# Kernel tuning notes

Hardware: AMD Instinct MI355X
Metric: run time of the kernel (lower is better)

## Reference

```python
import jax, jax.numpy as jnp
import numpy as np

NEG_INF = -9e15
ALPHA = 0.2  # LeakyReLU negative slope

N = 8192
D_IN = 512
D_OUT = 256


def setup_inputs() -> dict:
    key = jax.random.key(0)
    k1, k2, k3, k4, k5 = jax.random.split(key, 5)
    features = jax.random.normal(k1, (N, D_IN), dtype=jnp.float32)
    adjacency_matrix = jax.random.randint(k2, (N, N), 0, 2, dtype=jnp.int32)
    # learned params (torch Linear stores [out, in]; we use [in, out] layout)
    s_phi = 1.0 / np.sqrt(D_IN)
    W_phi = jax.random.uniform(k3, (D_IN, D_OUT), jnp.float32, -s_phi, s_phi)
    s_v = 1.0 / np.sqrt(D_OUT)
    w_mu = jax.random.uniform(k4, (D_OUT,), jnp.float32, -s_v, s_v)
    w_xi = jax.random.uniform(k5, (D_OUT,), jnp.float32, -s_v, s_v)
    return {"features": features, "adjacency_matrix": adjacency_matrix,
            "W_phi": W_phi, "w_mu": w_mu, "w_xi": w_xi}


def reference(features, adjacency_matrix, W_phi, w_mu, w_xi):
    h = features @ W_phi                                   # [N, d_out]
    mu = h @ w_mu                                          # [N]
    xi = h @ w_xi                                          # [N]
    e = mu[:, None] + xi[None, :]                          # [N, N] additive scores
    e = jnp.where(e >= 0, e, ALPHA * e)                    # LeakyReLU
    e = jnp.where(adjacency_matrix > 0, e, NEG_INF)        # mask non-edges
    a = jax.nn.softmax(e, axis=1)                          # row softmax (dropout p=0)
    out = a @ h                                            # weighted aggregation
    return jax.nn.elu(out)
```

## Files before the change

### kernel.cpp

```cpp
#include <hip/hip_runtime.h>
#include <cstdint>
#include <cstddef>


#define LOG2E 1.44269504f

typedef __attribute__((ext_vector_type(8))) short short8;
typedef __attribute__((ext_vector_type(4))) float floatx4;

using uint_as1 = __attribute__((address_space(1))) unsigned int;
using uint_as3 = __attribute__((address_space(3))) unsigned int;

__device__ __forceinline__ void gld_lds16(const void* g, void* l) {
  __builtin_amdgcn_global_load_lds((const uint_as1*)g, (uint_as3*)l, 16, 0, 0);
}

__device__ __forceinline__ unsigned short f2b(float f) {
  unsigned u = __float_as_uint(f);
  u += 0x7fffu + ((u >> 16) & 1u);
  return (unsigned short)(u >> 16);
}
__device__ __forceinline__ float b2f(short s) {
  return __uint_as_float(((unsigned)(unsigned short)s) << 16);
}

__global__ void k_bitmask(const int* __restrict__ adj, unsigned long long* __restrict__ bm) {
  int gw = (blockIdx.x * 256 + threadIdx.x) >> 6;
  int lane = threadIdx.x & 63;
  size_t w0 = (size_t)gw * 128;
  for (int r = 0; r < 128; r += 4) {
    size_t wd = w0 + r;
    int v0 = adj[(wd + 0) * 64 + lane];
    int v1 = adj[(wd + 1) * 64 + lane];
    int v2 = adj[(wd + 2) * 64 + lane];
    int v3 = adj[(wd + 3) * 64 + lane];
    unsigned long long m0 = __ballot(v0 != 0);
    unsigned long long m1 = __ballot(v1 != 0);
    unsigned long long m2 = __ballot(v2 != 0);
    unsigned long long m3 = __ballot(v3 != 0);
    if (lane == 0) {
      bm[wd] = m0; bm[wd + 1] = m1; bm[wd + 2] = m2; bm[wd + 3] = m3;
    }
  }
}

__global__ void k_cvt_features(const float* __restrict__ f, unsigned short* __restrict__ fb) {
  int tid = blockIdx.x * 256 + threadIdx.x;
  float4 v = ((const float4*)f)[tid];
  ushort4 o = {f2b(v.x), f2b(v.y), f2b(v.z), f2b(v.w)};
  *(ushort4*)&fb[tid * 4] = o;
}

__global__ void k_prep_wt(const float* __restrict__ w, unsigned short* __restrict__ wt) {
  int tid = blockIdx.x * 256 + threadIdx.x;
  int n = tid >> 9, k = tid & 511;
  wt[n * 512 + k] = f2b(w[k * 256 + n]);
}

__global__ void k_prep_p(const float* __restrict__ w, const float* __restrict__ wmu,
                         const float* __restrict__ wxi, float* __restrict__ pmu,
                         float* __restrict__ pxi) {
  int tid = blockIdx.x * 256 + threadIdx.x;
  int k = tid >> 2, seg = tid & 3;
  float sm = 0.f, sx = 0.f;
  int base = k * 256 + seg * 64;
#pragma unroll
  for (int c = 0; c < 64; c += 4) {
    float4 wv = *(const float4*)&w[base + c];
    float4 mv = *(const float4*)&wmu[seg * 64 + c];
    float4 xv = *(const float4*)&wxi[seg * 64 + c];
    sm += wv.x * mv.x + wv.y * mv.y + wv.z * mv.z + wv.w * mv.w;
    sx += wv.x * xv.x + wv.y * xv.y + wv.z * xv.z + wv.w * xv.w;
  }
  sm += __shfl_xor(sm, 1); sm += __shfl_xor(sm, 2);
  sx += __shfl_xor(sx, 1); sx += __shfl_xor(sx, 2);
  if (seg == 0) { pmu[k] = sm; pxi[k] = sx; }
}

__global__ void k_mu_xi(const unsigned short* __restrict__ fb, const float* __restrict__ pmu,
                        const float* __restrict__ pxi, float* __restrict__ mu,
                        float* __restrict__ xi) {
  int w = threadIdx.x >> 6, l = threadIdx.x & 63;
  int i = blockIdx.x * 4 + w;
  short8 fv = *(const short8*)&fb[i * 512 + l * 8];
  float m = 0.f, x = 0.f;
#pragma unroll
  for (int c = 0; c < 8; ++c) {
    float fvf = b2f(fv[c]);
    m = fmaf(fvf, pmu[l * 8 + c], m);
    x = fmaf(fvf, pxi[l * 8 + c], x);
  }
#pragma unroll
  for (int off = 32; off > 0; off >>= 1) {
    m += __shfl_xor(m, off);
    x += __shfl_xor(x, off);
  }
  if (l == 0) { mu[i] = m * LOG2E; xi[i] = x * LOG2E; }
}

__global__ __launch_bounds__(256, 2) void k_gemm1(const unsigned short* __restrict__ fb,
                                                  const unsigned short* __restrict__ wt,
                                                  unsigned short* __restrict__ ht) {
  __shared__ __align__(16) unsigned short As[64 * 64];
  __shared__ __align__(16) unsigned short Bs[128 * 64];
  int t = threadIdx.x, w = t >> 6, l = t & 63;
  int bm_ = blockIdx.x >> 1, bn = blockIdx.x & 1;
  int m0 = bm_ * 64, n0 = bn * 128;
  int lr = l >> 3, lg = l & 7, g = lg ^ lr;
  int kg = l >> 4, ln = l & 15;
  floatx4 zero = {0.f, 0.f, 0.f, 0.f};
  floatx4 acc[4][2];
#pragma unroll
  for (int mf = 0; mf < 4; ++mf)
#pragma unroll
    for (int nf = 0; nf < 2; ++nf) acc[mf][nf] = zero;

  for (int it = 0; it < 8; ++it) {
    int k0 = it * 64;
#pragma unroll
    for (int q = 0; q < 2; ++q) {
      int row = w * 16 + q * 8 + lr;
      const void* gp = fb + (size_t)(m0 + row) * 512 + k0 + g * 8;
      int lb = __builtin_amdgcn_readfirstlane((w * 16 + q * 8) * 64);
      gld_lds16(gp, &As[lb]);
    }
#pragma unroll
    for (int q = 0; q < 4; ++q) {
      int row = w * 32 + q * 8 + lr;
      const void* gp = wt + (size_t)(n0 + row) * 512 + k0 + g * 8;
      int lb = __builtin_amdgcn_readfirstlane((w * 32 + q * 8) * 64);
      gld_lds16(gp, &Bs[lb]);
    }
    __syncthreads();
#pragma unroll
    for (int ks = 0; ks < 2; ++ks) {
      int gg = ks * 4 + kg;
      int swz = (gg ^ (ln & 7)) * 8;
      short8 bfr[2];
#pragma unroll
      for (int nf = 0; nf < 2; ++nf)
        bfr[nf] = *(const short8*)&Bs[(w * 32 + nf * 16 + ln) * 64 + swz];
#pragma unroll
      for (int mf = 0; mf < 4; ++mf) {
        short8 afr = *(const short8*)&As[(mf * 16 + ln) * 64 + swz];
#pragma unroll
        for (int nf = 0; nf < 2; ++nf)
          acc[mf][nf] = __builtin_amdgcn_mfma_f32_16x16x32_bf16(afr, bfr[nf], acc[mf][nf], 0, 0, 0);
      }
    }
    __syncthreads();
  }
#pragma unroll
  for (int mf = 0; mf < 4; ++mf)
#pragma unroll
    for (int nf = 0; nf < 2; ++nf) {
      int ng = n0 + w * 32 + nf * 16 + ln;
      int mg = m0 + mf * 16 + kg * 4;
      ushort4 o = {f2b(acc[mf][nf][0]), f2b(acc[mf][nf][1]),
                   f2b(acc[mf][nf][2]), f2b(acc[mf][nf][3])};
      *(ushort4*)&ht[(size_t)ng * 8192 + mg] = o;
    }
}

__global__ void k_zero(float* __restrict__ num, float* __restrict__ zbuf) {
  int b = blockIdx.x, t = threadIdx.x;
  if (b < 2048) {
    float4 z4 = {0.f, 0.f, 0.f, 0.f};
    *(float4*)&num[(b * 256 + t) * 4] = z4;
  } else {
    zbuf[(b - 2048) * 256 + t] = 0.f;
  }
}

__global__ __launch_bounds__(256, 2) void k_attn5(const unsigned short* __restrict__ bm16,
                                                  const unsigned short* __restrict__ ht,
                                                  const float* __restrict__ mu,
                                                  const float* __restrict__ xi,
                                                  float* __restrict__ num,
                                                  float* __restrict__ zbuf) {
  __shared__ __align__(16) unsigned short Bs[2][256 * 64];
  __shared__ __align__(16) unsigned short Ws[64 * 64];

  int t = threadIdx.x, w = t >> 6, l = t & 63;
  int ln = l & 15, kg = l >> 4;
  int lr = l >> 3, lg = l & 7, g = lg ^ lr;
  int bi = blockIdx.x & 127, bj = blockIdx.x >> 7;
  int i0 = bi * 64;
  size_t jw = (size_t)bj * 2048;

  int wi = t >> 2;
  int js = (t & 3) * 16;
  int g0 = (t & 3) * 2;
  int p0i = (g0 ^ (wi & 7)) * 8;
  int p1i = ((g0 + 1) ^ (wi & 7)) * 8;
  float mu_s = mu[i0 + wi];
  const unsigned short* brow = bm16 + (size_t)(i0 + wi) * 512 + (jw + js) / 16;
  const float* xrow = xi + jw + js;
  float zacc = 0.f;

  floatx4 zero = {0.f, 0.f, 0.f, 0.f};
  floatx4 acc[4][4];
#pragma unroll
  for (int mf = 0; mf < 4; ++mf)
#pragma unroll
    for (int nf = 0; nf < 4; ++nf) acc[mf][nf] = zero;

  {
    unsigned bits = brow[0];
    float4 x0 = *(const float4*)(xrow + 0);
    float4 x1 = *(const float4*)(xrow + 4);
    float4 x2 = *(const float4*)(xrow + 8);
    float4 x3 = *(const float4*)(xrow + 12);
#pragma unroll
    for (int q = 0; q < 8; ++q) {
      int row = w * 64 + q * 8;
      const void* gp = ht + (size_t)(row + lr) * 8192 + jw + g * 8;
      int lb = __builtin_amdgcn_readfirstlane(row * 64);
      gld_lds16(gp, &Bs[0][lb]);
    }
    float xv[16] = {x0.x, x0.y, x0.z, x0.w, x1.x, x1.y, x1.z, x1.w,
                    x2.x, x2.y, x2.z, x2.w, x3.x, x3.y, x3.z, x3.w};
    short8 pk0, pk1;
#pragma unroll
    for (int e = 0; e < 16; ++e) {
      float s = mu_s + xv[e];
      s = fmaxf(s, 0.2f * s);
      float ev = __builtin_amdgcn_exp2f(s);
      float wv = (bits & (1u << e)) ? ev : 0.f;
      zacc += wv;
      if (e < 8) pk0[e] = (short)f2b(wv); else pk1[e - 8] = (short)f2b(wv);
    }
    *(short8*)&Ws[wi * 64 + p0i] = pk0;
    *(short8*)&Ws[wi * 64 + p1i] = pk1;
  }
  __syncthreads();

  for (int c = 0; c < 32; ++c) {
    int buf = c & 1, nb = buf ^ 1;
    float4 x0, x1, x2, x3;
    unsigned bits = 0;
    if (c < 31) {
      int jo1 = (c + 1) * 64;
#pragma unroll
      for (int q = 0; q < 8; ++q) {
        int row = w * 64 + q * 8;
        const void* gp = ht + (size_t)(row + lr) * 8192 + jw + jo1 + g * 8;
        int lb = __builtin_amdgcn_readfirstlane(nb * (256 * 64) + row * 64);
        gld_lds16(gp, &Bs[0][lb]);
      }
      bits = brow[(c + 1) * 4];
      x0 = *(const float4*)(xrow + jo1);
      x1 = *(const float4*)(xrow + jo1 + 4);
      x2 = *(const float4*)(xrow + jo1 + 8);
      x3 = *(const float4*)(xrow + jo1 + 12);
    }
#pragma unroll
    for (int ks = 0; ks < 2; ++ks) {
      int swz = ((ks * 4 + kg) ^ (ln & 7)) * 8;
      short8 af[4], bf[4];
#pragma unroll
      for (int mf = 0; mf < 4; ++mf)
        af[mf] = *(const short8*)&Ws[(mf * 16 + ln) * 64 + swz];
#pragma unroll
      for (int nf = 0; nf < 4; ++nf)
        bf[nf] = *(const short8*)&Bs[buf][(w * 64 + nf * 16 + ln) * 64 + swz];
#pragma unroll
      for (int mf = 0; mf < 4; ++mf)
#pragma unroll
        for (int nf = 0; nf < 4; ++nf)
          acc[mf][nf] = __builtin_amdgcn_mfma_f32_16x16x32_bf16(af[mf], bf[nf], acc[mf][nf], 0, 0, 0);
    }
    __syncthreads();
    if (c < 31) {
      float xv[16] = {x0.x, x0.y, x0.z, x0.w, x1.x, x1.y, x1.z, x1.w,
                      x2.x, x2.y, x2.z, x2.w, x3.x, x3.y, x3.z, x3.w};
      short8 pk0, pk1;
#pragma unroll
      for (int e = 0; e < 16; ++e) {
        float s = mu_s + xv[e];
        s = fmaxf(s, 0.2f * s);
        float ev = __builtin_amdgcn_exp2f(s);
        float wv = (bits & (1u << e)) ? ev : 0.f;
        zacc += wv;
        if (e < 8) pk0[e] = (short)f2b(wv); else pk1[e - 8] = (short)f2b(wv);
      }
      *(short8*)&Ws[wi * 64 + p0i] = pk0;
      *(short8*)&Ws[wi * 64 + p1i] = pk1;
    }
    __syncthreads();
  }

  zacc += __shfl_xor(zacc, 1);
  zacc += __shfl_xor(zacc, 2);
  if ((t & 3) == 0) atomicAdd(&zbuf[i0 + wi], zacc);

#pragma unroll
  for (int mf = 0; mf < 4; ++mf)
#pragma unroll
    for (int nf = 0; nf < 4; ++nf) {
      int col = w * 64 + nf * 16 + ln;
#pragma unroll
      for (int r = 0; r < 4; ++r) {
        int row = i0 + mf * 16 + kg * 4 + r;
        atomicAdd(&num[(size_t)row * 256 + col], acc[mf][nf][r]);
      }
    }
}

__global__ void k_final(const float* __restrict__ num, const float* __restrict__ zbuf,
                        float* __restrict__ out) {
  int tid = blockIdx.x * 256 + threadIdx.x;
  int i = tid >> 6;
  float zi = 1.0f / zbuf[i];
  float4 v = *(const float4*)&num[tid * 4];
  v.x *= zi; v.y *= zi; v.z *= zi; v.w *= zi;
  v.x = (v.x > 0.f) ? v.x : (__builtin_amdgcn_exp2f(v.x * LOG2E) - 1.f);
  v.y = (v.y > 0.f) ? v.y : (__builtin_amdgcn_exp2f(v.y * LOG2E) - 1.f);
  v.z = (v.z > 0.f) ? v.z : (__builtin_amdgcn_exp2f(v.z * LOG2E) - 1.f);
  v.w = (v.w > 0.f) ? v.w : (__builtin_amdgcn_exp2f(v.w * LOG2E) - 1.f);
  *(float4*)&out[tid * 4] = v;
}

extern "C" void kernel_launch(void* const* d_in, const int* in_sizes, int n_in,
                              void* d_out, int out_size, void* d_ws, size_t ws_size,
                              hipStream_t stream) {
  const float* features = (const float*)d_in[0];
  const int* adjm = (const int*)d_in[1];
  const float* W_phi = (const float*)d_in[2];
  const float* w_mu = (const float*)d_in[3];
  const float* w_xi = (const float*)d_in[4];
  float* out = (float*)d_out;

  char* ws = (char*)d_ws;
  unsigned short* fb  = (unsigned short*)(ws + 0);
  unsigned short* ht  = (unsigned short*)(ws + 8388608);
  unsigned short* wt  = (unsigned short*)(ws + 12582912);
  float* pmu = (float*)(ws + 12845056);
  float* pxi = (float*)(ws + 12847104);
  float* muv = (float*)(ws + 12849152);
  float* xiv = (float*)(ws + 12881920);
  unsigned long long* bmask = (unsigned long long*)(ws + 13631488);
  float* num  = (float*)(ws + 0);
  float* zbuf = (float*)(ws + 12582912);

  k_bitmask<<<2048, 256, 0, stream>>>(adjm, bmask);
  k_cvt_features<<<4096, 256, 0, stream>>>(features, fb);
  k_prep_wt<<<512, 256, 0, stream>>>(W_phi, wt);
  k_prep_p<<<8, 256, 0, stream>>>(W_phi, w_mu, w_xi, pmu, pxi);
  k_mu_xi<<<2048, 256, 0, stream>>>(fb, pmu, pxi, muv, xiv);
  k_gemm1<<<256, 256, 0, stream>>>(fb, wt, ht);
  k_zero<<<2080, 256, 0, stream>>>(num, zbuf);
  k_attn5<<<512, 256, 0, stream>>>((const unsigned short*)bmask, ht, muv, xiv, num, zbuf);
  k_final<<<2048, 256, 0, stream>>>(num, zbuf, out);
}
```

Baseline: 489.2 us.

## Factor exp of LeakyReLU scores into per-node products and drop atomics

Precomputes exp(mu), exp(0.2 mu), exp(xi) and exp(0.2 xi) per node. Each attention weight then becomes max(Emu*Exi, Fmu*Fxi), so the per-element exp disappears and the weights are built directly in MFMA A-fragments. The row-sum Z comes from an MFMA against a ones vector. Tiling changes to 256 rows by 128 columns over 1024-wide j chunks, and results go to per-chunk partial buffers reduced in k_final, which removes the zeroing kernel and the float atomics. In exchange it risks overflow or underflow without max subtraction, since the exponentials are computed separately before multiplying, and it adds more partial-buffer traffic.

```diff
diff --git a/kernel.cpp b/kernel.cpp
--- a/kernel.cpp
+++ b/kernel.cpp
@@ -78,8 +78,9 @@
 }
 
 __global__ void k_mu_xi(const unsigned short* __restrict__ fb, const float* __restrict__ pmu,
-                        const float* __restrict__ pxi, float* __restrict__ mu,
-                        float* __restrict__ xi) {
+                        const float* __restrict__ pxi, float* __restrict__ Emu,
+                        float* __restrict__ Fmu, float* __restrict__ Exi,
+                        float* __restrict__ Fxi) {
   int w = threadIdx.x >> 6, l = threadIdx.x & 63;
   int i = blockIdx.x * 4 + w;
   short8 fv = *(const short8*)&fb[i * 512 + l * 8];
@@ -95,7 +96,13 @@
     m += __shfl_xor(m, off);
     x += __shfl_xor(x, off);
   }
-  if (l == 0) { mu[i] = m * LOG2E; xi[i] = x * LOG2E; }
+  if (l == 0) {
+    float ms = m * LOG2E, xs = x * LOG2E;
+    Emu[i] = __builtin_amdgcn_exp2f(ms);
+    Fmu[i] = __builtin_amdgcn_exp2f(0.2f * ms);
+    Exi[i] = __builtin_amdgcn_exp2f(xs);
+    Fxi[i] = __builtin_amdgcn_exp2f(0.2f * xs);
+  }
 }
 
 __global__ __launch_bounds__(256, 2) void k_gemm1(const unsigned short* __restrict__ fb,
@@ -162,157 +169,141 @@
     }
 }
 
-__global__ void k_zero(float* __restrict__ num, float* __restrict__ zbuf) {
-  int b = blockIdx.x, t = threadIdx.x;
-  if (b < 2048) {
-    float4 z4 = {0.f, 0.f, 0.f, 0.f};
-    *(float4*)&num[(b * 256 + t) * 4] = z4;
-  } else {
-    zbuf[(b - 2048) * 256 + t] = 0.f;
-  }
-}
-
-__global__ __launch_bounds__(256, 2) void k_attn5(const unsigned short* __restrict__ bm16,
+__global__ __launch_bounds__(256, 2) void k_attn6(const unsigned char* __restrict__ bm8,
                                                   const unsigned short* __restrict__ ht,
-                                                  const float* __restrict__ mu,
-                                                  const float* __restrict__ xi,
-                                                  float* __restrict__ num,
-                                                  float* __restrict__ zbuf) {
-  __shared__ __align__(16) unsigned short Bs[2][256 * 64];
-  __shared__ __align__(16) unsigned short Ws[64 * 64];
+                                                  const float* __restrict__ Emu,
+                                                  const float* __restrict__ Fmu,
+                                                  const float* __restrict__ Exi,
+                                                  const float* __restrict__ Fxi,
+                                                  float* __restrict__ nump,
+                                                  float* __restrict__ zpart) {
+  __shared__ __align__(16) unsigned short Bs[128 * 256];
+  __shared__ __align__(16) unsigned char BitS[256 * 32];
+  __shared__ __align__(16) float ExiS[256];
+  __shared__ __align__(16) float FxiS[256];
 
   int t = threadIdx.x, w = t >> 6, l = t & 63;
   int ln = l & 15, kg = l >> 4;
-  int lr = l >> 3, lg = l & 7, g = lg ^ lr;
-  int bi = blockIdx.x & 127, bj = blockIdx.x >> 7;
-  int i0 = bi * 64;
-  size_t jw = (size_t)bj * 2048;
-
-  int wi = t >> 2;
-  int js = (t & 3) * 16;
-  int g0 = (t & 3) * 2;
-  int p0i = (g0 ^ (wi & 7)) * 8;
-  int p1i = ((g0 + 1) ^ (wi & 7)) * 8;
-  float mu_s = mu[i0 + wi];
-  const unsigned short* brow = bm16 + (size_t)(i0 + wi) * 512 + (jw + js) / 16;
-  const float* xrow = xi + jw + js;
-  float zacc = 0.f;
+  int b = blockIdx.x;
+  int ib = b & 31, nb = (b >> 5) & 1, jb = b >> 6;
+  int i0 = ib * 256, n0 = nb * 128;
+  int jbase = jb * 1024;
+
+  float emu[4], fmu[4];
+#pragma unroll
+  for (int mf = 0; mf < 4; ++mf) {
+    int i = i0 + w * 64 + mf * 16 + ln;
+    emu[mf] = Emu[i];
+    fmu[mf] = Fmu[i];
+  }
 
   floatx4 zero = {0.f, 0.f, 0.f, 0.f};
-  floatx4 acc[4][4];
+  floatx4 acc[4][8];
 #pragma unroll
   for (int mf = 0; mf < 4; ++mf)
 #pragma unroll
-    for (int nf = 0; nf < 4; ++nf) acc[mf][nf] = zero;
-
-  {
-    unsigned bits = brow[0];
-    float4 x0 = *(const float4*)(xrow + 0);
-    float4 x1 = *(const float4*)(xrow + 4);
-    float4 x2 = *(const float4*)(xrow + 8);
-    float4 x3 = *(const float4*)(xrow + 12);
-#pragma unroll
-    for (int q = 0; q < 8; ++q) {
-      int row = w * 64 + q * 8;
-      const void* gp = ht + (size_t)(row + lr) * 8192 + jw + g * 8;
-      int lb = __builtin_amdgcn_readfirstlane(row * 64);
-      gld_lds16(gp, &Bs[0][lb]);
-    }
-    float xv[16] = {x0.x, x0.y, x0.z, x0.w, x1.x, x1.y, x1.z, x1.w,
-                    x2.x, x2.y, x2.z, x2.w, x3.x, x3.y, x3.z, x3.w};
-    short8 pk0, pk1;
-#pragma unroll
-    for (int e = 0; e < 16; ++e) {
-      float s = mu_s + xv[e];
-      s = fmaxf(s, 0.2f * s);
-      float ev = __builtin_amdgcn_exp2f(s);
-      float wv = (bits & (1u << e)) ? ev : 0.f;
-      zacc += wv;
-      if (e < 8) pk0[e] = (short)f2b(wv); else pk1[e - 8] = (short)f2b(wv);
-    }
-    *(short8*)&Ws[wi * 64 + p0i] = pk0;
-    *(short8*)&Ws[wi * 64 + p1i] = pk1;
-  }
-  __syncthreads();
-
-  for (int c = 0; c < 32; ++c) {
-    int buf = c & 1, nb = buf ^ 1;
-    float4 x0, x1, x2, x3;
-    unsigned bits = 0;
-    if (c < 31) {
-      int jo1 = (c + 1) * 64;
-#pragma unroll
-      for (int q = 0; q < 8; ++q) {
-        int row = w * 64 + q * 8;
-        const void* gp = ht + (size_t)(row + lr) * 8192 + jw + jo1 + g * 8;
-        int lb = __builtin_amdgcn_readfirstlane(nb * (256 * 64) + row * 64);
-        gld_lds16(gp, &Bs[0][lb]);
+    for (int nf = 0; nf < 8; ++nf) acc[mf][nf] = zero;
+  floatx4 accz[4];
+#pragma unroll
+  for (int mf = 0; mf < 4; ++mf) accz[mf] = zero;
+
+  short8 ones;
+#pragma unroll
+  for (int e = 0; e < 8; ++e) ones[e] = (short)0x3F80;
+
+  for (int win = 0; win < 4; ++win) {
+    int jcol = jbase + win * 256;
+    __syncthreads();
+#pragma unroll
+    for (int q = 0; q < 16; ++q) {
+      int r0 = w * 32 + q * 2;
+      int rowl = r0 + (l >> 5);
+      int glog = (l & 31) ^ (rowl & 7);
+      const void* gp = ht + (size_t)(n0 + rowl) * 8192 + jcol + glog * 8;
+      int lb = __builtin_amdgcn_readfirstlane(r0 * 256);
+      gld_lds16(gp, &Bs[lb]);
+    }
+#pragma unroll
+    for (int q2 = 0; q2 < 2; ++q2) {
+      int r0 = w * 64 + q2 * 32;
+      int row = r0 + (l >> 1);
+      const void* gp = bm8 + (size_t)(i0 + row) * 1024 + (jcol >> 3) + (l & 1) * 16;
+      int lb = __builtin_amdgcn_readfirstlane(r0 * 32);
+      gld_lds16(gp, &BitS[lb]);
+    }
+    if (w == 2) gld_lds16(Exi + jcol + l * 4, &ExiS[0]);
+    if (w == 3) gld_lds16(Fxi + jcol + l * 4, &FxiS[0]);
+    __syncthreads();
+
+#pragma unroll
+    for (int ks = 0; ks < 8; ++ks) {
+      int gran = ks * 4 + kg;
+      int jo = gran * 8;
+      float4 e0 = *(const float4*)&ExiS[jo];
+      float4 e1 = *(const float4*)&ExiS[jo + 4];
+      float4 f0 = *(const float4*)&FxiS[jo];
+      float4 f1 = *(const float4*)&FxiS[jo + 4];
+      float ex[8] = {e0.x, e0.y, e0.z, e0.w, e1.x, e1.y, e1.z, e1.w};
+      float fx[8] = {f0.x, f0.y, f0.z, f0.w, f1.x, f1.y, f1.z, f1.w};
+      short8 af[4];
+#pragma unroll
+      for (int mf = 0; mf < 4; ++mf) {
+        unsigned bits = BitS[(w * 64 + mf * 16 + ln) * 32 + gran];
+        float A = emu[mf], F = fmu[mf];
+#pragma unroll
+        for (int e = 0; e < 8; ++e) {
+          float wv = fmaxf(A * ex[e], F * fx[e]);
+          wv = (bits & (1u << e)) ? wv : 0.f;
+          af[mf][e] = (short)f2b(wv);
+        }
       }
-      bits = brow[(c + 1) * 4];
-      x0 = *(const float4*)(xrow + jo1);
-      x1 = *(const float4*)(xrow + jo1 + 4);
-      x2 = *(const float4*)(xrow + jo1 + 8);
-      x3 = *(const float4*)(xrow + jo1 + 12);
-    }
-#pragma unroll
-    for (int ks = 0; ks < 2; ++ks) {
-      int swz = ((ks * 4 + kg) ^ (ln & 7)) * 8;
-      short8 af[4], bf[4];
 #pragma unroll
       for (int mf = 0; mf < 4; ++mf)
-        af[mf] = *(const short8*)&Ws[(mf * 16 + ln) * 64 + swz];
-#pragma unroll
-      for (int nf = 0; nf < 4; ++nf)
-        bf[nf] = *(const short8*)&Bs[buf][(w * 64 + nf * 16 + ln) * 64 + swz];
-#pragma unroll
-      for (int mf = 0; mf < 4; ++mf)
-#pragma unroll
-        for (int nf = 0; nf < 4; ++nf)
-          acc[mf][nf] = __builtin_amdgcn_mfma_f32_16x16x32_bf16(af[mf], bf[nf], acc[mf][nf], 0, 0, 0);
-    }
-    __syncthreads();
-    if (c < 31) {
-      float xv[16] = {x0.x, x0.y, x0.z, x0.w, x1.x, x1.y, x1.z, x1.w,
-                      x2.x, x2.y, x2.z, x2.w, x3.x, x3.y, x3.z, x3.w};
-      short8 pk0, pk1;
-#pragma unroll
-      for (int e = 0; e < 16; ++e) {
-        float s = mu_s + xv[e];
-        s = fmaxf(s, 0.2f * s);
-        float ev = __builtin_amdgcn_exp2f(s);
-        float wv = (bits & (1u << e)) ? ev : 0.f;
-        zacc += wv;
-        if (e < 8) pk0[e] = (short)f2b(wv); else pk1[e - 8] = (short)f2b(wv);
+        accz[mf] = __builtin_amdgcn_mfma_f32_16x16x32_bf16(af[mf], ones, accz[mf], 0, 0, 0);
+#pragma unroll
+      for (int nf = 0; nf < 8; ++nf) {
+        int nl = nf * 16 + ln;
+        short8 bf = *(const short8*)&Bs[nl * 256 + ((gran ^ (nl & 7)) * 8)];
+#pragma unroll
+        for (int mf = 0; mf < 4; ++mf)
+          acc[mf][nf] = __builtin_amdgcn_mfma_f32_16x16x32_bf16(af[mf], bf, acc[mf][nf], 0, 0, 0);
       }
-      *(short8*)&Ws[wi * 64 + p0i] = pk0;
-      *(short8*)&Ws[wi * 64 + p1i] = pk1;
-    }
-    __syncthreads();
-  }
-
-  zacc += __shfl_xor(zacc, 1);
-  zacc += __shfl_xor(zacc, 2);
-  if ((t & 3) == 0) atomicAdd(&zbuf[i0 + wi], zacc);
-
-#pragma unroll
-  for (int mf = 0; mf < 4; ++mf)
-#pragma unroll
-    for (int nf = 0; nf < 4; ++nf) {
-      int col = w * 64 + nf * 16 + ln;
-#pragma unroll
-      for (int r = 0; r < 4; ++r) {
-        int row = i0 + mf * 16 + kg * 4 + r;
-        atomicAdd(&num[(size_t)row * 256 + col], acc[mf][nf][r]);
-      }
-    }
-}
-
-__global__ void k_final(const float* __restrict__ num, const float* __restrict__ zbuf,
+    }
+  }
+
+  float* np = nump + (size_t)jb * (8192 * 256);
+#pragma unroll
+  for (int mf = 0; mf < 4; ++mf) {
+    int rowb = i0 + w * 64 + mf * 16 + kg * 4;
+#pragma unroll
+    for (int nf = 0; nf < 8; ++nf) {
+      int col = n0 + nf * 16 + ln;
+#pragma unroll
+      for (int r = 0; r < 4; ++r)
+        np[(size_t)(rowb + r) * 256 + col] = acc[mf][nf][r];
+    }
+    if (nb == 0 && ln == 0) {
+#pragma unroll
+      for (int r = 0; r < 4; ++r)
+        zpart[jb * 8192 + rowb + r] = accz[mf][r];
+    }
+  }
+}
+
+__global__ void k_final(const float* __restrict__ nump, const float* __restrict__ zpart,
                         float* __restrict__ out) {
   int tid = blockIdx.x * 256 + threadIdx.x;
   int i = tid >> 6;
-  float zi = 1.0f / zbuf[i];
-  float4 v = *(const float4*)&num[tid * 4];
+  float z = 0.f;
+#pragma unroll
+  for (int p = 0; p < 8; ++p) z += zpart[p * 8192 + i];
+  float zi = 1.0f / z;
+  float4 v = {0.f, 0.f, 0.f, 0.f};
+#pragma unroll
+  for (int p = 0; p < 8; ++p) {
+    float4 s = *(const float4*)&nump[(size_t)p * (8192 * 256) + tid * 4];
+    v.x += s.x; v.y += s.y; v.z += s.z; v.w += s.w;
+  }
   v.x *= zi; v.y *= zi; v.z *= zi; v.w *= zi;
   v.x = (v.x > 0.f) ? v.x : (__builtin_amdgcn_exp2f(v.x * LOG2E) - 1.f);
   v.y = (v.y > 0.f) ? v.y : (__builtin_amdgcn_exp2f(v.y * LOG2E) - 1.f);
@@ -337,19 +328,20 @@
   unsigned short* wt  = (unsigned short*)(ws + 12582912);
   float* pmu = (float*)(ws + 12845056);
   float* pxi = (float*)(ws + 12847104);
-  float* muv = (float*)(ws + 12849152);
-  float* xiv = (float*)(ws + 12881920);
-  unsigned long long* bmask = (unsigned long long*)(ws + 13631488);
-  float* num  = (float*)(ws + 0);
-  float* zbuf = (float*)(ws + 12582912);
-
-  k_bitmask<<<2048, 256, 0, stream>>>(adjm, bmask);
+  float* Emu = (float*)(ws + 12849152);
+  float* Fmu = (float*)(ws + 12881920);
+  float* Exi = (float*)(ws + 12914688);
+  float* Fxi = (float*)(ws + 12947456);
+  unsigned char* bmask = (unsigned char*)(ws + 13631488);
+  float* zpart = (float*)(ws + 22020096);
+  float* nump  = (float*)(ws + 25165824);
+
+  k_bitmask<<<2048, 256, 0, stream>>>(adjm, (unsigned long long*)bmask);
   k_cvt_features<<<4096, 256, 0, stream>>>(features, fb);
   k_prep_wt<<<512, 256, 0, stream>>>(W_phi, wt);
   k_prep_p<<<8, 256, 0, stream>>>(W_phi, w_mu, w_xi, pmu, pxi);
-  k_mu_xi<<<2048, 256, 0, stream>>>(fb, pmu, pxi, muv, xiv);
+  k_mu_xi<<<2048, 256, 0, stream>>>(fb, pmu, pxi, Emu, Fmu, Exi, Fxi);
   k_gemm1<<<256, 256, 0, stream>>>(fb, wt, ht);
-  k_zero<<<2080, 256, 0, stream>>>(num, zbuf);
-  k_attn5<<<512, 256, 0, stream>>>((const unsigned short*)bmask, ht, muv, xiv, num, zbuf);
-  k_final<<<2048, 256, 0, stream>>>(num, zbuf, out);
-}
+  k_attn6<<<512, 256, 0, stream>>>(bmask, ht, Emu, Fmu, Exi, Fxi, nump, zpart);
+  k_final<<<2048, 256, 0, stream>>>(nump, zpart, out);
+}
```

Result: no change. 497.9 us (+1.8%).
